# Kernel optimization log

Hardware: AMD Instinct MI355X
Metric: run time of the kernel (lower is better)

The kernel has to match this reference:

```python
import jax, jax.numpy as jnp
import numpy as np

HEAD_SIZE = 64
EMBED = 512


def setup_inputs() -> dict:
    key = jax.random.key(0)
    kx, kk, kq, kv = jax.random.split(key, 4)
    x = jax.random.normal(kx, (4, 4096, EMBED), dtype=jnp.float32)
    # torch Linear(EMBED, HEAD_SIZE, bias=False) weight: [HEAD_SIZE, EMBED]
    scale = 1.0 / np.sqrt(EMBED)
    Wk = jax.random.normal(kk, (HEAD_SIZE, EMBED), dtype=jnp.float32) * scale
    Wq = jax.random.normal(kq, (HEAD_SIZE, EMBED), dtype=jnp.float32) * scale
    Wv = jax.random.normal(kv, (HEAD_SIZE, EMBED), dtype=jnp.float32) * scale
    return {"x": x, "Wk": Wk, "Wq": Wq, "Wv": Wv}


def reference(x, Wk, Wq, Wv):
    B, T, C = x.shape
    # projections: x @ W.T  -> [B, T, H]
    k = jnp.einsum('btc,hc->bth', x, Wk)
    q = jnp.einsum('btc,hc->bth', x, Wq)
    v = jnp.einsum('btc,hc->bth', x, Wv)
    # scores scaled by C**-0.5 (input embed dim, as in the source module)
    scores = jnp.einsum('bth,bsh->bts', q, k) * (C ** -0.5)  # [B, T, T]
    causal = jnp.tril(jnp.ones((T, T), dtype=bool))
    scores = jnp.where(causal, scores, -jnp.inf)
    weights = jax.nn.softmax(scores, axis=-1)
    # dropout p=0.0 -> identity
    out = jnp.einsum('bts,bsh->bth', weights, v)  # [B, T, H]
    return out
```

## Files before the change

kernel.cpp:

```cpp
#include <hip/hip_runtime.h>

typedef unsigned short u16;
typedef unsigned int   u32;

#define NB 4
#define NT 4096
#define NC 512
#define NH 64
#define ATT_SCALE 0.044194173824159216f
#define LOG2E     1.4426950408889634f
#define QSCALE    (ATT_SCALE * LOG2E)
#define NEG_BIG   -30000.0f
#define ITEMS_PB  1088
#define ITEMS2_PB 2176

typedef __attribute__((ext_vector_type(8))) _Float16 half8;
typedef __attribute__((ext_vector_type(4))) _Float16 half4;
typedef __attribute__((ext_vector_type(4))) float    floatx4;


__global__ __launch_bounds__(256) void wconv(
    const float* __restrict__ Wk, const float* __restrict__ Wq,
    const float* __restrict__ Wv, _Float16* __restrict__ Wh)
{
    const int gid = blockIdx.x * 256 + threadIdx.x;
    const int w = gid >> 13;
    const int i = gid & 8191;
    const int h = i >> 7, c = (i & 127) * 4;
    const float* src = (w == 0) ? Wq : (w == 1) ? Wk : Wv;
    const float sc = (w == 0) ? QSCALE : 1.0f;
    float4 f = *(const float4*)&src[h * NC + c];
    half4 o = {(_Float16)(f.x * sc), (_Float16)(f.y * sc),
               (_Float16)(f.z * sc), (_Float16)(f.w * sc)};
    const int blk = ((w * 16 + (c >> 5)) * 4 + (h >> 4));
    *(half4*)&Wh[(size_t)blk * 512 + (h & 15) * 32 + ((c >> 3) & 3) * 8 + (c & 7)] = o;
}

__global__ __launch_bounds__(256) void qkv_mfma(
    const float* __restrict__ x, const _Float16* __restrict__ Wh,
    _Float16* __restrict__ Qf, _Float16* __restrict__ Kf,
    _Float16* __restrict__ Vf)
{
    __shared__ __align__(16) floatx4 red[3][12][64];

    const int tid  = threadIdx.x;
    const int wv   = tid >> 6;
    const int lane = tid & 63;
    const int quad = lane >> 4;
    const int id   = lane & 15;
    const int rowbase = blockIdx.x * 16;

    floatx4 acc[3][4] = {};
    const float* xp = x + (size_t)(rowbase + id) * NC + wv * 128;
    const int loff = id * 32 + quad * 8;

    float4 xr[8];
#pragma unroll
    for (int ksq = 0; ksq < 8; ++ksq)
        xr[ksq] = *(const float4*)&xp[(ksq >> 1) * 32 + quad * 8 + (ksq & 1) * 4];

#pragma unroll
    for (int ks = 0; ks < 4; ++ks) {
        float4 f0 = xr[2 * ks];
        float4 f1 = xr[2 * ks + 1];
        half8 a;
        a[0] = (_Float16)f0.x; a[1] = (_Float16)f0.y;
        a[2] = (_Float16)f0.z; a[3] = (_Float16)f0.w;
        a[4] = (_Float16)f1.x; a[5] = (_Float16)f1.y;
        a[6] = (_Float16)f1.z; a[7] = (_Float16)f1.w;
        const int ksg = wv * 4 + ks;
#pragma unroll
        for (int w = 0; w < 3; ++w)
#pragma unroll
            for (int nt = 0; nt < 4; ++nt) {
                half8 bf = *(const half8*)&Wh[(size_t)((w * 16 + ksg) * 4 + nt) * 512 + loff];
                acc[w][nt] = __builtin_amdgcn_mfma_f32_16x16x32_f16(a, bf, acc[w][nt], 0, 0, 0);
            }
    }

#pragma unroll
    for (int idx = 0; idx < 12; ++idx) {
        const int ow = idx / 3;
        if (ow != wv)
            red[(wv > ow) ? wv - 1 : wv][idx][lane] = acc[idx >> 2][idx & 3];
    }
    __syncthreads();

    const int b  = rowbase >> 12, L = rowbase & 4095;
    const int q16 = L >> 4, kt = L >> 6, tt = (L >> 4) & 3;
    const int kop = ((rowbase & 63) + quad * 4) >> 5;
    const int q4k = ((((rowbase & 63) + quad * 4) >> 3) & 3);

#define QKV_EPIL(IDX) do {                                                     \
    constexpr int w_ = (IDX) >> 2, nt_ = (IDX) & 3;                            \
    floatx4 a_ = acc[w_][nt_];                                                 \
    a_ += red[0][IDX][lane] + red[1][IDX][lane] + red[2][IDX][lane];           \
    if (w_ == 0 || w_ == 1) {                                                  \
        const int hop = nt_ >> 1;                                              \
        const int q4h = (nt_ * 2 + (id >> 3)) & 3;                             \
        const int j   = id & 7;                                                \
        const size_t ad = (w_ == 0)                                            \
            ? (size_t)((b * 256 + q16) * 2 + hop) * 512 + q4h * 8 + j          \
            : (size_t)(((b * 64 + kt) * 4 + tt) * 2 + hop) * 512 + q4h * 8 + j;\
        _Float16* dstp = (w_ == 0) ? Qf : Kf;                                  \
        _Pragma("unroll")                                                      \
        for (int r = 0; r < 4; ++r)                                            \
            dstp[ad + (quad * 4 + r) * 32] = (_Float16)a_[r];                  \
    } else {                                                                   \
        half4 vh = {(_Float16)a_[0], (_Float16)a_[1],                          \
                    (_Float16)a_[2], (_Float16)a_[3]};                         \
        const size_t va = (size_t)(((b * 64 + kt) * 4 + nt_) * 2 + kop) * 512  \
                        + id * 32 + q4k * 8 + (quad & 1) * 4;                  \
        *(half4*)&Vf[va] = vh;                                                 \
    }                                                                          \
} while (0)

    if (wv == 0)      { QKV_EPIL(0); QKV_EPIL(1);  QKV_EPIL(2);  }
    else if (wv == 1) { QKV_EPIL(3); QKV_EPIL(4);  QKV_EPIL(5);  }
    else if (wv == 2) { QKV_EPIL(6); QKV_EPIL(7);  QKV_EPIL(8);  }
    else              { QKV_EPIL(9); QKV_EPIL(10); QKV_EPIL(11); }
#undef QKV_EPIL
}

__global__ __launch_bounds__(256, 4) void attn_part(
    const _Float16* __restrict__ Qf, const _Float16* __restrict__ Kf,
    const _Float16* __restrict__ Vf, _Float16* __restrict__ Opart,
    float2* __restrict__ MLpart)
{
    constexpr int KP = 72;
    __shared__ __align__(16) _Float16 Ps[4][16 * KP];

    const int tid  = threadIdx.x;
    const int wv   = tid >> 6;
    const int lane = tid & 63;
    const int quad = lane >> 4;
    const int id   = lane & 15;
    const int item2 = blockIdx.x * 4 + wv;
    const int item  = item2 >> 1;
    const int st    = item2 & 1;
    const int b     = blockIdx.y;
    const int loff  = id * 32 + quad * 8;

    int m = (int)((1.0f + __builtin_sqrtf((float)item + 1.0f)) * 0.5f);
    while (4 * m * (m + 1) <= item) ++m;
    while (m > 1 && 4 * m * (m - 1) > item) --m;
    const int rem  = item - 4 * m * (m - 1);
    const int qs   = 8 * (m - 1) + rem / m;
    const int seg  = rem - (rem / m) * m;
    const int ntiles = (qs >> 1) + 1;
    const int t0 = seg * ntiles / m;
    const int t1 = (seg + 1) * ntiles / m;

    const size_t qa = (size_t)((b * 256 + qs * 2 + st) * 2) * 512 + loff;
    const half8 qb0 = *(const half8*)&Qf[qa];
    const half8 qb1 = *(const half8*)&Qf[qa + 512];

    floatx4 o[4] = {};
    float m_i = NEG_BIG;
    float l_q = 0.f;

    size_t tb = (size_t)((b * 64 + t0) * 8) * 512 + loff;
    half8 kc[8], kn[8], vc[8];
#pragma unroll
    for (int t = 0; t < 8; ++t) kc[t] = *(const half8*)&Kf[tb + (size_t)t * 512];

    for (int kt = t0; kt < t1; ++kt) {
#pragma unroll
        for (int t = 0; t < 8; ++t) vc[t] = *(const half8*)&Vf[tb + (size_t)t * 512];
        const bool more = (kt + 1 < t1);
        if (more) {
#pragma unroll
            for (int t = 0; t < 8; ++t)
                kn[t] = *(const half8*)&Kf[tb + 4096 + (size_t)t * 512];
        }

        floatx4 s4[4] = {};
#pragma unroll
        for (int t = 0; t < 4; ++t) {
            s4[t] = __builtin_amdgcn_mfma_f32_16x16x32_f16(kc[2 * t],     qb0, s4[t], 0, 0, 0);
            s4[t] = __builtin_amdgcn_mfma_f32_16x16x32_f16(kc[2 * t + 1], qb1, s4[t], 0, 0, 0);
        }

        if (kt == ntiles - 1) {
            const int kb = kt * 64;
            const int qrow = qs * 32 + st * 16 + id;
#pragma unroll
            for (int t = 0; t < 4; ++t)
#pragma unroll
                for (int r = 0; r < 4; ++r)
                    if (kb + 16 * t + quad * 4 + r > qrow)
                        s4[t][r] = NEG_BIG;
        }

        float pmax = s4[0][0];
#pragma unroll
        for (int t = 0; t < 4; ++t)
#pragma unroll
            for (int r = 0; r < 4; ++r) pmax = fmaxf(pmax, s4[t][r]);

        if (__any(pmax > m_i + 8.0f)) {
            float mx = pmax;
            mx = fmaxf(mx, __shfl_xor(mx, 16));
            mx = fmaxf(mx, __shfl_xor(mx, 32));
            const float mnew  = fmaxf(m_i, mx);
            const float alpha = exp2f(m_i - mnew);
            m_i = mnew;
            l_q *= alpha;
#pragma unroll
            for (int t = 0; t < 4; ++t)
#pragma unroll
                for (int r = 0; r < 4; ++r) o[t][r] *= alpha;
        }

        float psum = 0.f;
#pragma unroll
        for (int t = 0; t < 4; ++t)
#pragma unroll
            for (int r = 0; r < 4; ++r) {
                const float p = exp2f(s4[t][r] - m_i);
                s4[t][r] = p;
                psum += p;
            }
        l_q += psum;

#pragma unroll
        for (int t = 0; t < 4; ++t) {
            half4 ph = {(_Float16)s4[t][0], (_Float16)s4[t][1],
                        (_Float16)s4[t][2], (_Float16)s4[t][3]};
            *(half4*)&Ps[wv][id * KP + 16 * t + quad * 4] = ph;
        }
        const half8 pb0 = *(const half8*)&Ps[wv][id * KP + quad * 8];
        const half8 pb1 = *(const half8*)&Ps[wv][id * KP + 32 + quad * 8];

#pragma unroll
        for (int t = 0; t < 4; ++t) {
            o[t] = __builtin_amdgcn_mfma_f32_16x16x32_f16(vc[2 * t],     pb0, o[t], 0, 0, 0);
            o[t] = __builtin_amdgcn_mfma_f32_16x16x32_f16(vc[2 * t + 1], pb1, o[t], 0, 0, 0);
        }

        if (more) {
#pragma unroll
            for (int t = 0; t < 8; ++t) kc[t] = kn[t];
        }
        tb += 4096;
    }

    float l_t = l_q;
    l_t += __shfl_xor(l_t, 16);
    l_t += __shfl_xor(l_t, 32);

    const int p = b * ITEMS2_PB + item2;
    const float rl = 1.f / l_t;
#pragma unroll
    for (int t = 0; t < 4; ++t) {
        half4 oh = {(_Float16)(o[t][0] * rl), (_Float16)(o[t][1] * rl),
                    (_Float16)(o[t][2] * rl), (_Float16)(o[t][3] * rl)};
        *(half4*)&Ps[wv][id * KP + 16 * t + quad * 4] = oh;
    }
    const int rr = lane >> 3, rc = (lane & 7) * 8;
    half8 u0 = *(const half8*)&Ps[wv][rr * KP + rc];
    half8 u1 = *(const half8*)&Ps[wv][(8 + rr) * KP + rc];
    _Float16* ob = &Opart[(size_t)(p * 16) * NH];
    *(half8*)&ob[rr * NH + rc] = u0;
    *(half8*)&ob[(8 + rr) * NH + rc] = u1;

    if (quad == 0)
        MLpart[p * 16 + id] = make_float2(m_i, l_t);
}

__global__ __launch_bounds__(256) void attn_combine(
    const _Float16* __restrict__ Opart, const float2* __restrict__ MLpart,
    float* __restrict__ out)
{
    const int qs = blockIdx.x, b = blockIdx.y;
    const int tid = threadIdx.x;
    const int row = tid >> 3;
    const int hc  = tid & 7;
    const int sst = row >> 4, r16 = row & 15;
    const int m = (qs >> 3) + 1;
    const int base0 = 4 * m * (m - 1) + (qs - 8 * (m - 1)) * m;

    auto gidx = [&](int k) -> size_t {
        return (size_t)(b * ITEMS2_PB + (base0 + k) * 2 + sst) * 16 + r16;
    };

    float2 ml[16];
#pragma unroll
    for (int k = 0; k < 16; ++k)
        ml[k] = MLpart[gidx(k < m ? k : 0)];

    float M = NEG_BIG;
#pragma unroll
    for (int k = 0; k < 16; ++k)
        if (k < m) M = fmaxf(M, ml[k].x);

    float w[16], W = 0.f;
#pragma unroll
    for (int k = 0; k < 16; ++k) {
        const float wk = (k < m) ? ml[k].y * exp2f(ml[k].x - M) : 0.f;
        w[k] = wk; W += wk;
    }

    float acc[8] = {};
#pragma unroll
    for (int k = 0; k < 16; ++k) {
        const half8 oh = *(const half8*)&Opart[gidx(k < m ? k : 0) * NH + hc * 8];
#pragma unroll
        for (int j = 0; j < 8; ++j) acc[j] += w[k] * (float)oh[j];
    }

    const float rl = 1.f / W;
    float* dst = out + (size_t)(b * NT + qs * 32 + row) * NH + hc * 8;
#pragma unroll
    for (int j = 0; j < 8; ++j) dst[j] = acc[j] * rl;
}

extern "C" void kernel_launch(void* const* d_in, const int* in_sizes, int n_in,
                              void* d_out, int out_size, void* d_ws, size_t ws_size,
                              hipStream_t stream) {
    const float* x  = (const float*)d_in[0];
    const float* Wk = (const float*)d_in[1];
    const float* Wq = (const float*)d_in[2];
    const float* Wv = (const float*)d_in[3];

    char* wsb = (char*)d_ws;
    _Float16* Qf    = (_Float16*)wsb;
    _Float16* Kf    = Qf + 1048576;
    _Float16* Vf    = Kf + 1048576;
    _Float16* Wh    = Vf + 1048576;
    float2*   MLpart= (float2*)(wsb + 6488064);
    _Float16* Opart = (_Float16*)(wsb + 7602176);

    wconv<<<96, 256, 0, stream>>>(Wk, Wq, Wv, Wh);
    qkv_mfma<<<1024, 256, 0, stream>>>(x, Wh, Qf, Kf, Vf);
    attn_part<<<dim3(ITEMS2_PB / 4, NB), 256, 0, stream>>>(Qf, Kf, Vf, Opart, MLpart);
    attn_combine<<<dim3(128, NB), 256, 0, stream>>>(Opart, MLpart, (float*)d_out);
}
```

Measured before the change: 149.8 us.

## Share K/V tiles across four waves via LDS with async double-buffered loads

```diff
diff --git a/kernel.cpp b/kernel.cpp
--- a/kernel.cpp
+++ b/kernel.cpp
@@ -11,12 +11,17 @@
 #define LOG2E     1.4426950408889634f
 #define QSCALE    (ATT_SCALE * LOG2E)
 #define NEG_BIG   -30000.0f
-#define ITEMS_PB  1088
-#define ITEMS2_PB 2176
+#define ITEMS3_PB 288
 
 typedef __attribute__((ext_vector_type(8))) _Float16 half8;
 typedef __attribute__((ext_vector_type(4))) _Float16 half4;
 typedef __attribute__((ext_vector_type(4))) float    floatx4;
+
+__device__ __forceinline__ void gload_lds16(const _Float16* g, _Float16* l) {
+    __builtin_amdgcn_global_load_lds(
+        (const __attribute__((address_space(1))) void*)g,
+        (__attribute__((address_space(3))) void*)l, 16, 0, 0);
+}
 
 
 __global__ __launch_bounds__(256) void wconv(
@@ -122,12 +127,13 @@
 #undef QKV_EPIL
 }
 
-__global__ __launch_bounds__(256, 4) void attn_part(
+__global__ __launch_bounds__(256) void attn_part(
     const _Float16* __restrict__ Qf, const _Float16* __restrict__ Kf,
     const _Float16* __restrict__ Vf, _Float16* __restrict__ Opart,
     float2* __restrict__ MLpart)
 {
     constexpr int KP = 72;
+    __shared__ __align__(16) _Float16 KV[2][2][4096];
     __shared__ __align__(16) _Float16 Ps[4][16 * KP];
 
     const int tid  = threadIdx.x;
@@ -135,62 +141,75 @@
     const int lane = tid & 63;
     const int quad = lane >> 4;
     const int id   = lane & 15;
-    const int item2 = blockIdx.x * 4 + wv;
-    const int item  = item2 >> 1;
-    const int st    = item2 & 1;
-    const int b     = blockIdx.y;
-    const int loff  = id * 32 + quad * 8;
-
-    int m = (int)((1.0f + __builtin_sqrtf((float)item + 1.0f)) * 0.5f);
-    while (4 * m * (m + 1) <= item) ++m;
-    while (m > 1 && 4 * m * (m - 1) > item) --m;
-    const int rem  = item - 4 * m * (m - 1);
-    const int qs   = 8 * (m - 1) + rem / m;
-    const int seg  = rem - (rem / m) * m;
-    const int ntiles = (qs >> 1) + 1;
-    const int t0 = seg * ntiles / m;
-    const int t1 = (seg + 1) * ntiles / m;
-
-    const size_t qa = (size_t)((b * 256 + qs * 2 + st) * 2) * 512 + loff;
+    const int b    = blockIdx.y;
+    const int item = (ITEMS3_PB - 1) - blockIdx.x;
+    const int loff = id * 32 + quad * 8;
+
+    int g = (int)(0.5f * (__builtin_sqrtf((float)item + 1.0f) - 1.0f));
+    while (4 * (g + 1) * (g + 2) <= item) ++g;
+    while (g > 0 && 4 * g * (g + 1) > item) --g;
+    const int rem = item - 4 * g * (g + 1);
+    const int np  = g + 1;
+    const int qb  = 8 * g + rem / np;
+    const int seg = rem - (rem / np) * np;
+    const int ntl = qb + 1;
+    const int t0 = seg * ntl / np, t1 = (seg + 1) * ntl / np;
+
+    const size_t qa = (size_t)((b * 256 + qb * 4 + wv) * 2) * 512 + loff;
     const half8 qb0 = *(const half8*)&Qf[qa];
     const half8 qb1 = *(const half8*)&Qf[qa + 512];
+
+    size_t gk = (size_t)((b * 64 + t0) * 8) * 512;
+    const int c0 = 2 * wv, c1 = 2 * wv + 1;
+
+    gload_lds16(&Kf[gk + (size_t)c0 * 512 + loff], &KV[0][0][c0 * 512]);
+    gload_lds16(&Kf[gk + (size_t)c1 * 512 + loff], &KV[0][0][c1 * 512]);
+    gload_lds16(&Vf[gk + (size_t)c0 * 512 + loff], &KV[0][1][c0 * 512]);
+    gload_lds16(&Vf[gk + (size_t)c1 * 512 + loff], &KV[0][1][c1 * 512]);
 
     floatx4 o[4] = {};
     float m_i = NEG_BIG;
     float l_q = 0.f;
 
-    size_t tb = (size_t)((b * 64 + t0) * 8) * 512 + loff;
-    half8 kc[8], kn[8], vc[8];
-#pragma unroll
-    for (int t = 0; t < 8; ++t) kc[t] = *(const half8*)&Kf[tb + (size_t)t * 512];
-
+    asm volatile("s_waitcnt vmcnt(0)" ::: "memory");
+    __syncthreads();
+
+    int cur = 0;
     for (int kt = t0; kt < t1; ++kt) {
-#pragma unroll
-        for (int t = 0; t < 8; ++t) vc[t] = *(const half8*)&Vf[tb + (size_t)t * 512];
         const bool more = (kt + 1 < t1);
         if (more) {
-#pragma unroll
-            for (int t = 0; t < 8; ++t)
-                kn[t] = *(const half8*)&Kf[tb + 4096 + (size_t)t * 512];
-        }
+            const size_t gn = gk + 4096;
+            gload_lds16(&Kf[gn + (size_t)c0 * 512 + loff], &KV[cur ^ 1][0][c0 * 512]);
+            gload_lds16(&Kf[gn + (size_t)c1 * 512 + loff], &KV[cur ^ 1][0][c1 * 512]);
+            gload_lds16(&Vf[gn + (size_t)c0 * 512 + loff], &KV[cur ^ 1][1][c0 * 512]);
+            gload_lds16(&Vf[gn + (size_t)c1 * 512 + loff], &KV[cur ^ 1][1][c1 * 512]);
+        }
+        const _Float16* Kc = &KV[cur][0][0];
+        const _Float16* Vc = &KV[cur][1][0];
 
         floatx4 s4[4] = {};
 #pragma unroll
         for (int t = 0; t < 4; ++t) {
-            s4[t] = __builtin_amdgcn_mfma_f32_16x16x32_f16(kc[2 * t],     qb0, s4[t], 0, 0, 0);
-            s4[t] = __builtin_amdgcn_mfma_f32_16x16x32_f16(kc[2 * t + 1], qb1, s4[t], 0, 0, 0);
-        }
-
-        if (kt == ntiles - 1) {
-            const int kb = kt * 64;
-            const int qrow = qs * 32 + st * 16 + id;
+            const half8 k0 = *(const half8*)&Kc[(size_t)(2 * t)     * 512 + lane * 8];
+            const half8 k1 = *(const half8*)&Kc[(size_t)(2 * t + 1) * 512 + lane * 8];
+            s4[t] = __builtin_amdgcn_mfma_f32_16x16x32_f16(k0, qb0, s4[t], 0, 0, 0);
+            s4[t] = __builtin_amdgcn_mfma_f32_16x16x32_f16(k1, qb1, s4[t], 0, 0, 0);
+        }
+
+        if (kt == qb) {
+            const int qrow = wv * 16 + id;
 #pragma unroll
             for (int t = 0; t < 4; ++t)
 #pragma unroll
                 for (int r = 0; r < 4; ++r)
-                    if (kb + 16 * t + quad * 4 + r > qrow)
+                    if (16 * t + quad * 4 + r > qrow)
                         s4[t][r] = NEG_BIG;
         }
+
+        half8 vf[8];
+#pragma unroll
+        for (int c = 0; c < 8; ++c)
+            vf[c] = *(const half8*)&Vc[(size_t)c * 512 + lane * 8];
 
         float pmax = s4[0][0];
 #pragma unroll
@@ -234,22 +253,22 @@
 
 #pragma unroll
         for (int t = 0; t < 4; ++t) {
-            o[t] = __builtin_amdgcn_mfma_f32_16x16x32_f16(vc[2 * t],     pb0, o[t], 0, 0, 0);
-            o[t] = __builtin_amdgcn_mfma_f32_16x16x32_f16(vc[2 * t + 1], pb1, o[t], 0, 0, 0);
-        }
-
-        if (more) {
-#pragma unroll
-            for (int t = 0; t < 8; ++t) kc[t] = kn[t];
-        }
-        tb += 4096;
+            o[t] = __builtin_amdgcn_mfma_f32_16x16x32_f16(vf[2 * t],     pb0, o[t], 0, 0, 0);
+            o[t] = __builtin_amdgcn_mfma_f32_16x16x32_f16(vf[2 * t + 1], pb1, o[t], 0, 0, 0);
+        }
+
+        if (more)
+            asm volatile("s_waitcnt vmcnt(0)" ::: "memory");
+        __syncthreads();
+        cur ^= 1;
+        gk += 4096;
     }
 
     float l_t = l_q;
     l_t += __shfl_xor(l_t, 16);
     l_t += __shfl_xor(l_t, 32);
 
-    const int p = b * ITEMS2_PB + item2;
+    const int p = b * ITEMS3_PB + item;
     const float rl = 1.f / l_t;
 #pragma unroll
     for (int t = 0; t < 4; ++t) {
@@ -260,57 +279,62 @@
     const int rr = lane >> 3, rc = (lane & 7) * 8;
     half8 u0 = *(const half8*)&Ps[wv][rr * KP + rc];
     half8 u1 = *(const half8*)&Ps[wv][(8 + rr) * KP + rc];
-    _Float16* ob = &Opart[(size_t)(p * 16) * NH];
+    _Float16* ob = &Opart[((size_t)p * 64 + wv * 16) * NH];
     *(half8*)&ob[rr * NH + rc] = u0;
     *(half8*)&ob[(8 + rr) * NH + rc] = u1;
 
     if (quad == 0)
-        MLpart[p * 16 + id] = make_float2(m_i, l_t);
+        MLpart[(size_t)p * 64 + wv * 16 + id] = make_float2(m_i, l_t);
 }
 
 __global__ __launch_bounds__(256) void attn_combine(
     const _Float16* __restrict__ Opart, const float2* __restrict__ MLpart,
     float* __restrict__ out)
 {
-    const int qs = blockIdx.x, b = blockIdx.y;
+    const int b   = blockIdx.y;
     const int tid = threadIdx.x;
-    const int row = tid >> 3;
+    const int row = blockIdx.x * 32 + (tid >> 3);
     const int hc  = tid & 7;
-    const int sst = row >> 4, r16 = row & 15;
-    const int m = (qs >> 3) + 1;
-    const int base0 = 4 * m * (m - 1) + (qs - 8 * (m - 1)) * m;
+    const int qb  = row >> 6;
+    const int rin = row & 63;
+    const int g   = qb >> 3;
+    const int m   = g + 1;
+    const int base = 4 * g * (g + 1) + (qb & 7) * m;
 
     auto gidx = [&](int k) -> size_t {
-        return (size_t)(b * ITEMS2_PB + (base0 + k) * 2 + sst) * 16 + r16;
+        return ((size_t)b * ITEMS3_PB + base + k) * 64 + rin;
     };
 
-    float2 ml[16];
-#pragma unroll
-    for (int k = 0; k < 16; ++k)
+    float2 ml[8];
+#pragma unroll
+    for (int k = 0; k < 8; ++k)
         ml[k] = MLpart[gidx(k < m ? k : 0)];
 
+    half8 ohv[8];
+#pragma unroll
+    for (int k = 0; k < 8; ++k)
+        ohv[k] = *(const half8*)&Opart[gidx(k < m ? k : 0) * NH + hc * 8];
+
     float M = NEG_BIG;
 #pragma unroll
-    for (int k = 0; k < 16; ++k)
+    for (int k = 0; k < 8; ++k)
         if (k < m) M = fmaxf(M, ml[k].x);
 
-    float w[16], W = 0.f;
-#pragma unroll
-    for (int k = 0; k < 16; ++k) {
+    float w[8], W = 0.f;
+#pragma unroll
+    for (int k = 0; k < 8; ++k) {
         const float wk = (k < m) ? ml[k].y * exp2f(ml[k].x - M) : 0.f;
         w[k] = wk; W += wk;
     }
 
     float acc[8] = {};
 #pragma unroll
-    for (int k = 0; k < 16; ++k) {
-        const half8 oh = *(const half8*)&Opart[gidx(k < m ? k : 0) * NH + hc * 8];
-#pragma unroll
-        for (int j = 0; j < 8; ++j) acc[j] += w[k] * (float)oh[j];
-    }
+    for (int k = 0; k < 8; ++k)
+#pragma unroll
+        for (int j = 0; j < 8; ++j) acc[j] += w[k] * (float)ohv[k][j];
 
     const float rl = 1.f / W;
-    float* dst = out + (size_t)(b * NT + qs * 32 + row) * NH + hc * 8;
+    float* dst = out + (size_t)(b * NT + row) * NH + hc * 8;
 #pragma unroll
     for (int j = 0; j < 8; ++j) dst[j] = acc[j] * rl;
 }
@@ -333,6 +357,6 @@
 
     wconv<<<96, 256, 0, stream>>>(Wk, Wq, Wv, Wh);
     qkv_mfma<<<1024, 256, 0, stream>>>(x, Wh, Qf, Kf, Vf);
-    attn_part<<<dim3(ITEMS2_PB / 4, NB), 256, 0, stream>>>(Qf, Kf, Vf, Opart, MLpart);
+    attn_part<<<dim3(ITEMS3_PB, NB), 256, 0, stream>>>(Qf, Kf, Vf, Opart, MLpart);
     attn_combine<<<dim3(128, NB), 256, 0, stream>>>(Opart, MLpart, (float*)d_out);
 }
```

Measured after the change: 124.9 us. 16.6% less time.
